# Optimization experiments

Hardware: AMD Instinct MI355X
Metric: run time of the kernel (lower is better)

The kernel has to match this reference:

```python
import jax, jax.numpy as jnp
import numpy as np

NUM_HEADS = 32
NEG_INF = -1e9


def setup_inputs() -> dict:
    key = jax.random.key(0)
    ks = jax.random.split(key, 7)
    B, S, H = 8, 4, 4096
    hd = H // NUM_HEADS
    position = 4096
    max_seq = position + S  # 4100
    sc = H ** -0.5  # keep projection outputs O(1)
    return {
        "hidden_states": jax.random.normal(ks[0], (B, S, H), jnp.float32),
        "Wq": jax.random.normal(ks[1], (H, H), jnp.float32) * sc,
        "Wk": jax.random.normal(ks[2], (H, H), jnp.float32) * sc,
        "Wv": jax.random.normal(ks[3], (H, H), jnp.float32) * sc,
        "Wo": jax.random.normal(ks[4], (H, H), jnp.float32) * sc,
        "key_cache": jax.random.normal(ks[5], (B, NUM_HEADS, max_seq, hd), jnp.float32),
        "value_cache": jax.random.normal(ks[6], (B, NUM_HEADS, max_seq, hd), jnp.float32),
        "position": position,
    }


def reference(hidden_states, Wq, Wk, Wv, Wo, key_cache, value_cache, position):
    B, S, H = hidden_states.shape
    nh = NUM_HEADS
    hd = H // nh
    scale = hd ** -0.5

    def proj(x, W):  # nn.Linear: x @ W.T -> [B, nh, S, hd]
        return (x @ W.T).reshape(B, S, nh, hd).transpose(0, 2, 1, 3)

    q = proj(hidden_states, Wq)
    k = proj(hidden_states, Wk)
    v = proj(hidden_states, Wv)

    # KV-cache slice update (position is a static Python int)
    key_cache = jax.lax.dynamic_update_slice(key_cache, k, (0, 0, position, 0))
    value_cache = jax.lax.dynamic_update_slice(value_cache, v, (0, 0, position, 0))

    kv_len = position + S
    k_all = key_cache[:, :, :kv_len, :]   # [B, nh, kv_len, hd]
    v_all = value_cache[:, :, :kv_len, :]

    scores = jnp.einsum('bhsd,bhtd->bhst', q, k_all) * scale  # [B, nh, S, kv_len]
    # triu(ones(S, kv_len), diagonal=position+1): mask col t when t > position + s
    mask = jnp.arange(kv_len)[None, :] > (position + jnp.arange(S))[:, None]
    scores = jnp.where(mask, NEG_INF, scores)
    attn = jax.nn.softmax(scores, axis=-1)

    out = jnp.einsum('bhst,bhtd->bhsd', attn, v_all)
    out = out.transpose(0, 2, 1, 3).reshape(B, S, H)
    return out @ Wo.T
```

## Files before the change

### kernel.cpp

```cpp
#include <hip/hip_runtime.h>
#include <cstdint>

#define HDIM   4096
#define NHEADS 32
#define HDH    128
#define BB     8
#define SQ     4
#define MAXSEQ 4100
#define QSCALE 0.08838834764831845f

#define PKCH  64
#define PLSTR 68
#define KSPL  512

__device__ __forceinline__ void dot4(float& a, const float4& p, const float4& q) {
    a = fmaf(p.x, q.x, fmaf(p.y, q.y, fmaf(p.z, q.z, fmaf(p.w, q.w, a))));
}

__global__ __launch_bounds__(256) void proj_split(
    const float* __restrict__ X,
    const float* __restrict__ W0, const float* __restrict__ W1, const float* __restrict__ W2,
    float* __restrict__ P)
{
    __shared__ float Wt[128][PLSTR];
    __shared__ float Xt[32][PLSTR];
    const float* __restrict__ W = (blockIdx.z == 0) ? W0 : ((blockIdx.z == 1) ? W1 : W2);
    const int tid = threadIdx.x;
    const int c0 = blockIdx.x * 128;
    const int kbase = blockIdx.y * KSPL;
    const int cg = tid & 31;
    const int rg = tid >> 5;

    float acc[4][4];
    #pragma unroll
    for (int r = 0; r < 4; ++r)
        #pragma unroll
        for (int j = 0; j < 4; ++j) acc[r][j] = 0.f;

    for (int ch = 0; ch < KSPL; ch += PKCH) {
        const int k0 = kbase + ch;
        #pragma unroll
        for (int i = 0; i < 8; ++i) {
            int fidx = (i << 8) + tid;
            int row = fidx >> 4;
            int kq = (fidx & 15) << 2;
            *(float4*)&Wt[row][kq] = *(const float4*)&W[(size_t)(c0 + row) * HDIM + k0 + kq];
        }
        #pragma unroll
        for (int i = 0; i < 2; ++i) {
            int fidx = (i << 8) + tid;
            int row = fidx >> 4;
            int kq = (fidx & 15) << 2;
            *(float4*)&Xt[row][kq] = *(const float4*)&X[(size_t)row * HDIM + k0 + kq];
        }
        __syncthreads();
        #pragma unroll 4
        for (int k = 0; k < PKCH; k += 4) {
            float4 w0 = *(const float4*)&Wt[cg][k];
            float4 w1 = *(const float4*)&Wt[cg + 32][k];
            float4 w2 = *(const float4*)&Wt[cg + 64][k];
            float4 w3 = *(const float4*)&Wt[cg + 96][k];
            float4 x0 = *(const float4*)&Xt[rg * 4 + 0][k];
            float4 x1 = *(const float4*)&Xt[rg * 4 + 1][k];
            float4 x2 = *(const float4*)&Xt[rg * 4 + 2][k];
            float4 x3 = *(const float4*)&Xt[rg * 4 + 3][k];
            dot4(acc[0][0], x0, w0); dot4(acc[0][1], x0, w1); dot4(acc[0][2], x0, w2); dot4(acc[0][3], x0, w3);
            dot4(acc[1][0], x1, w0); dot4(acc[1][1], x1, w1); dot4(acc[1][2], x1, w2); dot4(acc[1][3], x1, w3);
            dot4(acc[2][0], x2, w0); dot4(acc[2][1], x2, w1); dot4(acc[2][2], x2, w2); dot4(acc[2][3], x2, w3);
            dot4(acc[3][0], x3, w0); dot4(acc[3][1], x3, w1); dot4(acc[3][2], x3, w2); dot4(acc[3][3], x3, w3);
        }
        __syncthreads();
    }

    float* __restrict__ Pp = P + (size_t)(blockIdx.z * gridDim.y + blockIdx.y) * 32 * HDIM;
    #pragma unroll
    for (int r = 0; r < 4; ++r)
        #pragma unroll
        for (int j = 0; j < 4; ++j)
            Pp[(size_t)(rg * 4 + r) * HDIM + c0 + j * 32 + cg] = acc[r][j];
}

__global__ __launch_bounds__(256) void reduce_qkv(
    const float* __restrict__ P, float* __restrict__ qw,
    float* __restrict__ kw, float* __restrict__ vw)
{
    const int idx = blockIdx.x * 256 + threadIdx.x;
    const int mat = idx >> 17;
    const int rc = idx & 131071;
    const float* p = P + (size_t)mat * 1048576 + rc;
    float s = 0.f;
    #pragma unroll
    for (int i = 0; i < 8; ++i) s += p[(size_t)i * 131072];
    const int r = rc >> 12, c = rc & 4095;
    const int b = r >> 2, si = r & 3, h = c >> 7, d = c & 127;
    const size_t o = ((size_t)(b * NHEADS + h) * SQ + si) * HDH + d;
    if (mat == 0)      qw[o] = s * QSCALE;
    else if (mat == 1) kw[o] = s;
    else               vw[o] = s;
}

__global__ __launch_bounds__(256) void reduce_out(
    const float* __restrict__ P, float* __restrict__ out)
{
    const int idx = blockIdx.x * 256 + threadIdx.x;
    float s = 0.f;
    #pragma unroll
    for (int i = 0; i < 8; ++i) s += P[(size_t)i * 131072 + idx];
    out[idx] = s;
}

__device__ __forceinline__ float tree_reduce4(float p0, float p1, float p2, float p3, int li) {
    float a = (li & 16) ? p1 : p0;
    float b = (li & 16) ? p0 : p1;
    a += __shfl_xor(b, 16);
    float c = (li & 16) ? p3 : p2;
    float d = (li & 16) ? p2 : p3;
    c += __shfl_xor(d, 16);
    float e = (li & 8) ? c : a;
    float f = (li & 8) ? a : c;
    e += __shfl_xor(f, 8);
    e += __shfl_xor(e, 4);
    e += __shfl_xor(e, 2);
    e += __shfl_xor(e, 1);
    return e;
}

__global__ __launch_bounds__(1024) void attn_kernel(
    const float* __restrict__ kc, const float* __restrict__ vc,
    const float* __restrict__ qw, const float* __restrict__ kw,
    const float* __restrict__ vw, float* __restrict__ ow,
    const int* __restrict__ posp)
{
    __shared__ __align__(16) float sc[MAXSEQ * 4];
    __shared__ __align__(16) float o_part[16][SQ][HDH];
    __shared__ float wmax[16][4];
    __shared__ float l_part[16][4];
    __shared__ float m_fin[4], l_fin[4];

    const int bh = blockIdx.x;
    const int pos = *posp;
    const int kvlen = pos + SQ;
    const int pos_main = pos & ~31;
    const int tid = threadIdx.x;
    const int w = tid >> 6;
    const int lane = tid & 63;
    const int half = (lane >> 5) & 1;
    const int li = lane & 31;
    const int sg = ((li >> 3) & 1) * 2 + ((li >> 4) & 1);

    const float* __restrict__ qb = qw + (size_t)bh * 512 + li * 4;
    const float4 q0 = *(const float4*)(qb + 0);
    const float4 q1 = *(const float4*)(qb + 128);
    const float4 q2 = *(const float4*)(qb + 256);
    const float4 q3 = *(const float4*)(qb + 384);

    const float* __restrict__ kbase = kc + (size_t)bh * MAXSEQ * HDH + li * 4;
    const float* __restrict__ vbase = vc + (size_t)bh * MAXSEQ * HDH + li * 4;
    const float* __restrict__ knew = kw + (size_t)bh * 512 + li * 4;
    const float* __restrict__ vnew = vw + (size_t)bh * 512 + li * 4;

    float mloc = -1e30f;

    {
        int t = 2 * w + half;
        if (t < pos_main) {
            float4 kcur = *(const float4*)(kbase + (size_t)t * HDH);
            while (true) {
                const int tn = t + 32;
                const bool more = (tn < pos_main);
                float4 knx;
                if (more) knx = *(const float4*)(kbase + (size_t)tn * HDH);
                float p0 = fmaf(q0.x, kcur.x, fmaf(q0.y, kcur.y, fmaf(q0.z, kcur.z, q0.w * kcur.w)));
                float p1 = fmaf(q1.x, kcur.x, fmaf(q1.y, kcur.y, fmaf(q1.z, kcur.z, q1.w * kcur.w)));
                float p2 = fmaf(q2.x, kcur.x, fmaf(q2.y, kcur.y, fmaf(q2.z, kcur.z, q2.w * kcur.w)));
                float p3 = fmaf(q3.x, kcur.x, fmaf(q3.y, kcur.y, fmaf(q3.z, kcur.z, q3.w * kcur.w)));
                float e = tree_reduce4(p0, p1, p2, p3, li);
                mloc = fmaxf(mloc, e);
                if ((li & 7) == 0) sc[t * 4 + sg] = e;
                if (!more) break;
                kcur = knx; t = tn;
            }
        }
        for (int tt = pos_main + 2 * w + half; tt < kvlen; tt += 32) {
            const float* kr = (tt < pos) ? (kbase + (size_t)tt * HDH)
                                         : (knew + (size_t)(tt - pos) * HDH);
            float4 k4 = *(const float4*)kr;
            float p0 = fmaf(q0.x, k4.x, fmaf(q0.y, k4.y, fmaf(q0.z, k4.z, q0.w * k4.w)));
            float p1 = fmaf(q1.x, k4.x, fmaf(q1.y, k4.y, fmaf(q1.z, k4.z, q1.w * k4.w)));
            float p2 = fmaf(q2.x, k4.x, fmaf(q2.y, k4.y, fmaf(q2.z, k4.z, q2.w * k4.w)));
            float p3 = fmaf(q3.x, k4.x, fmaf(q3.y, k4.y, fmaf(q3.z, k4.z, q3.w * k4.w)));
            float e = tree_reduce4(p0, p1, p2, p3, li);
            if (tt > pos + sg) e = -1e9f;
            mloc = fmaxf(mloc, e);
            if ((li & 7) == 0) sc[tt * 4 + sg] = e;
        }
    }
    float mw = fmaxf(mloc, __shfl_xor(mloc, 32));
    if (lane < 32 && (li & 7) == 0) wmax[w][sg] = mw;
    __syncthreads();
    if (tid < 4) {
        float m = wmax[0][tid];
        #pragma unroll
        for (int i = 1; i < 16; ++i) m = fmaxf(m, wmax[i][tid]);
        m_fin[tid] = m;
    }
    __syncthreads();
    const float mf0 = m_fin[0], mf1 = m_fin[1], mf2 = m_fin[2], mf3 = m_fin[3];

    float lp0 = 0.f, lp1 = 0.f, lp2 = 0.f, lp3 = 0.f;
    for (int t = tid; t < kvlen; t += 1024) {
        float4 s4 = *(float4*)&sc[t * 4];
        s4.x = __expf(s4.x - mf0);
        s4.y = __expf(s4.y - mf1);
        s4.z = __expf(s4.z - mf2);
        s4.w = __expf(s4.w - mf3);
        *(float4*)&sc[t * 4] = s4;
        lp0 += s4.x; lp1 += s4.y; lp2 += s4.z; lp3 += s4.w;
    }
    #pragma unroll
    for (int off = 32; off; off >>= 1) {
        lp0 += __shfl_xor(lp0, off);
        lp1 += __shfl_xor(lp1, off);
        lp2 += __shfl_xor(lp2, off);
        lp3 += __shfl_xor(lp3, off);
    }
    if (lane == 0) { l_part[w][0] = lp0; l_part[w][1] = lp1; l_part[w][2] = lp2; l_part[w][3] = lp3; }
    __syncthreads();
    if (tid < 4) {
        float L = 0.f;
        #pragma unroll
        for (int i = 0; i < 16; ++i) L += l_part[i][tid];
        l_fin[tid] = L;
    }

    float4 o0 = {0,0,0,0}, o1 = {0,0,0,0}, o2 = {0,0,0,0}, o3 = {0,0,0,0};
    {
        int t = 2 * w + half;
        if (t < pos_main) {
            float4 vcur = *(const float4*)(vbase + (size_t)t * HDH);
            while (true) {
                const int tn = t + 32;
                const bool more = (tn < pos_main);
                float4 vnx;
                if (more) vnx = *(const float4*)(vbase + (size_t)tn * HDH);
                float4 e4 = *(float4*)&sc[t * 4];
                o0.x = fmaf(e4.x, vcur.x, o0.x); o0.y = fmaf(e4.x, vcur.y, o0.y);
                o0.z = fmaf(e4.x, vcur.z, o0.z); o0.w = fmaf(e4.x, vcur.w, o0.w);
                o1.x = fmaf(e4.y, vcur.x, o1.x); o1.y = fmaf(e4.y, vcur.y, o1.y);
                o1.z = fmaf(e4.y, vcur.z, o1.z); o1.w = fmaf(e4.y, vcur.w, o1.w);
                o2.x = fmaf(e4.z, vcur.x, o2.x); o2.y = fmaf(e4.z, vcur.y, o2.y);
                o2.z = fmaf(e4.z, vcur.z, o2.z); o2.w = fmaf(e4.z, vcur.w, o2.w);
                o3.x = fmaf(e4.w, vcur.x, o3.x); o3.y = fmaf(e4.w, vcur.y, o3.y);
                o3.z = fmaf(e4.w, vcur.z, o3.z); o3.w = fmaf(e4.w, vcur.w, o3.w);
                if (!more) break;
                vcur = vnx; t = tn;
            }
        }
        for (int tt = pos_main + 2 * w + half; tt < kvlen; tt += 32) {
            const float* vr = (tt < pos) ? (vbase + (size_t)tt * HDH)
                                         : (vnew + (size_t)(tt - pos) * HDH);
            float4 v4 = *(const float4*)vr;
            float4 e4 = *(float4*)&sc[tt * 4];
            o0.x = fmaf(e4.x, v4.x, o0.x); o0.y = fmaf(e4.x, v4.y, o0.y);
            o0.z = fmaf(e4.x, v4.z, o0.z); o0.w = fmaf(e4.x, v4.w, o0.w);
            o1.x = fmaf(e4.y, v4.x, o1.x); o1.y = fmaf(e4.y, v4.y, o1.y);
            o1.z = fmaf(e4.y, v4.z, o1.z); o1.w = fmaf(e4.y, v4.w, o1.w);
            o2.x = fmaf(e4.z, v4.x, o2.x); o2.y = fmaf(e4.z, v4.y, o2.y);
            o2.z = fmaf(e4.z, v4.z, o2.z); o2.w = fmaf(e4.z, v4.w, o2.w);
            o3.x = fmaf(e4.w, v4.x, o3.x); o3.y = fmaf(e4.w, v4.y, o3.y);
            o3.z = fmaf(e4.w, v4.z, o3.z); o3.w = fmaf(e4.w, v4.w, o3.w);
        }
    }
    o0.x += __shfl_xor(o0.x, 32); o0.y += __shfl_xor(o0.y, 32);
    o0.z += __shfl_xor(o0.z, 32); o0.w += __shfl_xor(o0.w, 32);
    o1.x += __shfl_xor(o1.x, 32); o1.y += __shfl_xor(o1.y, 32);
    o1.z += __shfl_xor(o1.z, 32); o1.w += __shfl_xor(o1.w, 32);
    o2.x += __shfl_xor(o2.x, 32); o2.y += __shfl_xor(o2.y, 32);
    o2.z += __shfl_xor(o2.z, 32); o2.w += __shfl_xor(o2.w, 32);
    o3.x += __shfl_xor(o3.x, 32); o3.y += __shfl_xor(o3.y, 32);
    o3.z += __shfl_xor(o3.z, 32); o3.w += __shfl_xor(o3.w, 32);
    if (half == 0) {
        *(float4*)&o_part[w][0][li * 4] = o0;
        *(float4*)&o_part[w][1][li * 4] = o1;
        *(float4*)&o_part[w][2][li * 4] = o2;
        *(float4*)&o_part[w][3][li * 4] = o3;
    }
    __syncthreads();
    if (tid < 512) {
        const int s = tid >> 7, d = tid & 127;
        float a = 0.f;
        #pragma unroll
        for (int i = 0; i < 16; ++i) a += o_part[i][s][d];
        const int b = bh >> 5, h = bh & 31;
        ow[((size_t)(b * SQ + s) << 12) + (h << 7) + d] = a / l_fin[s];
    }
}

extern "C" void kernel_launch(void* const* d_in, const int* in_sizes, int n_in,
                              void* d_out, int out_size, void* d_ws, size_t ws_size,
                              hipStream_t stream) {
    const float* hs = (const float*)d_in[0];
    const float* Wq = (const float*)d_in[1];
    const float* Wk = (const float*)d_in[2];
    const float* Wv = (const float*)d_in[3];
    const float* Wo = (const float*)d_in[4];
    const float* kc = (const float*)d_in[5];
    const float* vc = (const float*)d_in[6];
    const int*  pos = (const int*)d_in[7];
    float* out = (float*)d_out;

    float* ws = (float*)d_ws;
    float* qw = ws;
    float* kw = ws + 131072;
    float* vw = ws + 262144;
    float* ow = ws + 393216;
    float* Pq = ws + 524288;
    float* Po = ws + 3670016;

    proj_split<<<dim3(32, 8, 3), 256, 0, stream>>>(hs, Wq, Wk, Wv, Pq);
    reduce_qkv<<<1536, 256, 0, stream>>>(Pq, qw, kw, vw);
    attn_kernel<<<256, 1024, 0, stream>>>(kc, vc, qw, kw, vw, ow, pos);
    proj_split<<<dim3(32, 8, 1), 256, 0, stream>>>(ow, Wo, Wo, Wo, Po);
    reduce_out<<<512, 256, 0, stream>>>(Po, out);
}
```

Measured before the change: 339.6 us.

## Fuse QKV split-K reduction into attention kernel and deepen KV prefetch

Removes the separate reduce_qkv launch. Each attention block now sums the eight split-K partials for its own head's q, k and v directly from the projection workspace into shared memory, and the new k/v rows are read from LDS instead of global buffers. It also changes the K and V streaming loops from a one-ahead to a two-ahead register prefetch to hide more memory latency. This saves a launch and the round trip of writing and re-reading q/k/v. In exchange it adds extra LDS, register pressure and a serial reduction prologue at the start of every attention block.

```diff
diff --git a/kernel.cpp b/kernel.cpp
--- a/kernel.cpp
+++ b/kernel.cpp
@@ -80,25 +80,6 @@
             Pp[(size_t)(rg * 4 + r) * HDIM + c0 + j * 32 + cg] = acc[r][j];
 }
 
-__global__ __launch_bounds__(256) void reduce_qkv(
-    const float* __restrict__ P, float* __restrict__ qw,
-    float* __restrict__ kw, float* __restrict__ vw)
-{
-    const int idx = blockIdx.x * 256 + threadIdx.x;
-    const int mat = idx >> 17;
-    const int rc = idx & 131071;
-    const float* p = P + (size_t)mat * 1048576 + rc;
-    float s = 0.f;
-    #pragma unroll
-    for (int i = 0; i < 8; ++i) s += p[(size_t)i * 131072];
-    const int r = rc >> 12, c = rc & 4095;
-    const int b = r >> 2, si = r & 3, h = c >> 7, d = c & 127;
-    const size_t o = ((size_t)(b * NHEADS + h) * SQ + si) * HDH + d;
-    if (mat == 0)      qw[o] = s * QSCALE;
-    else if (mat == 1) kw[o] = s;
-    else               vw[o] = s;
-}
-
 __global__ __launch_bounds__(256) void reduce_out(
     const float* __restrict__ P, float* __restrict__ out)
 {
@@ -127,12 +108,14 @@
 
 __global__ __launch_bounds__(1024) void attn_kernel(
     const float* __restrict__ kc, const float* __restrict__ vc,
-    const float* __restrict__ qw, const float* __restrict__ kw,
-    const float* __restrict__ vw, float* __restrict__ ow,
+    const float* __restrict__ Pq, float* __restrict__ ow,
     const int* __restrict__ posp)
 {
     __shared__ __align__(16) float sc[MAXSEQ * 4];
     __shared__ __align__(16) float o_part[16][SQ][HDH];
+    __shared__ __align__(16) float qs_lds[SQ * HDH];
+    __shared__ __align__(16) float ks_lds[SQ * HDH];
+    __shared__ __align__(16) float vs_lds[SQ * HDH];
     __shared__ float wmax[16][4];
     __shared__ float l_part[16][4];
     __shared__ float m_fin[4], l_fin[4];
@@ -148,43 +131,64 @@
     const int li = lane & 31;
     const int sg = ((li >> 3) & 1) * 2 + ((li >> 4) & 1);
 
-    const float* __restrict__ qb = qw + (size_t)bh * 512 + li * 4;
-    const float4 q0 = *(const float4*)(qb + 0);
-    const float4 q1 = *(const float4*)(qb + 128);
-    const float4 q2 = *(const float4*)(qb + 256);
-    const float4 q3 = *(const float4*)(qb + 384);
+    {
+        const int b = bh >> 5, h = bh & 31;
+        if (tid < 512) {
+            const int s = tid >> 7, d = tid & 127;
+            const size_t base = (size_t)(b * SQ + s) * HDIM + h * HDH + d;
+            float a = 0.f;
+            #pragma unroll
+            for (int i = 0; i < 8; ++i) a += Pq[(size_t)i * 131072 + base];
+            qs_lds[tid] = a * QSCALE;
+        } else {
+            const int u = tid - 512;
+            const int s = u >> 7, d = u & 127;
+            const size_t base = (size_t)(b * SQ + s) * HDIM + h * HDH + d;
+            float ak = 0.f, av = 0.f;
+            #pragma unroll
+            for (int i = 0; i < 8; ++i) {
+                ak += Pq[(size_t)(8 + i) * 131072 + base];
+                av += Pq[(size_t)(16 + i) * 131072 + base];
+            }
+            ks_lds[u] = ak;
+            vs_lds[u] = av;
+        }
+    }
+    __syncthreads();
+
+    const float4 q0 = *(const float4*)&qs_lds[0 * HDH + li * 4];
+    const float4 q1 = *(const float4*)&qs_lds[1 * HDH + li * 4];
+    const float4 q2 = *(const float4*)&qs_lds[2 * HDH + li * 4];
+    const float4 q3 = *(const float4*)&qs_lds[3 * HDH + li * 4];
 
     const float* __restrict__ kbase = kc + (size_t)bh * MAXSEQ * HDH + li * 4;
     const float* __restrict__ vbase = vc + (size_t)bh * MAXSEQ * HDH + li * 4;
-    const float* __restrict__ knew = kw + (size_t)bh * 512 + li * 4;
-    const float* __restrict__ vnew = vw + (size_t)bh * 512 + li * 4;
 
     float mloc = -1e30f;
 
     {
-        int t = 2 * w + half;
-        if (t < pos_main) {
-            float4 kcur = *(const float4*)(kbase + (size_t)t * HDH);
-            while (true) {
-                const int tn = t + 32;
-                const bool more = (tn < pos_main);
-                float4 knx;
-                if (more) knx = *(const float4*)(kbase + (size_t)tn * HDH);
-                float p0 = fmaf(q0.x, kcur.x, fmaf(q0.y, kcur.y, fmaf(q0.z, kcur.z, q0.w * kcur.w)));
-                float p1 = fmaf(q1.x, kcur.x, fmaf(q1.y, kcur.y, fmaf(q1.z, kcur.z, q1.w * kcur.w)));
-                float p2 = fmaf(q2.x, kcur.x, fmaf(q2.y, kcur.y, fmaf(q2.z, kcur.z, q2.w * kcur.w)));
-                float p3 = fmaf(q3.x, kcur.x, fmaf(q3.y, kcur.y, fmaf(q3.z, kcur.z, q3.w * kcur.w)));
+        const int t0 = 2 * w + half;
+        if (t0 < pos_main) {
+            float4 ka = *(const float4*)(kbase + (size_t)t0 * HDH);
+            float4 kb;
+            if (t0 + 32 < pos_main) kb = *(const float4*)(kbase + (size_t)(t0 + 32) * HDH);
+            for (int t = t0; t < pos_main; t += 32) {
+                float4 kn;
+                if (t + 64 < pos_main) kn = *(const float4*)(kbase + (size_t)(t + 64) * HDH);
+                float p0 = fmaf(q0.x, ka.x, fmaf(q0.y, ka.y, fmaf(q0.z, ka.z, q0.w * ka.w)));
+                float p1 = fmaf(q1.x, ka.x, fmaf(q1.y, ka.y, fmaf(q1.z, ka.z, q1.w * ka.w)));
+                float p2 = fmaf(q2.x, ka.x, fmaf(q2.y, ka.y, fmaf(q2.z, ka.z, q2.w * ka.w)));
+                float p3 = fmaf(q3.x, ka.x, fmaf(q3.y, ka.y, fmaf(q3.z, ka.z, q3.w * ka.w)));
                 float e = tree_reduce4(p0, p1, p2, p3, li);
                 mloc = fmaxf(mloc, e);
                 if ((li & 7) == 0) sc[t * 4 + sg] = e;
-                if (!more) break;
-                kcur = knx; t = tn;
+                ka = kb; kb = kn;
             }
         }
         for (int tt = pos_main + 2 * w + half; tt < kvlen; tt += 32) {
-            const float* kr = (tt < pos) ? (kbase + (size_t)tt * HDH)
-                                         : (knew + (size_t)(tt - pos) * HDH);
-            float4 k4 = *(const float4*)kr;
+            float4 k4;
+            if (tt < pos) k4 = *(const float4*)(kbase + (size_t)tt * HDH);
+            else          k4 = *(const float4*)&ks_lds[(tt - pos) * HDH + li * 4];
             float p0 = fmaf(q0.x, k4.x, fmaf(q0.y, k4.y, fmaf(q0.z, k4.z, q0.w * k4.w)));
             float p1 = fmaf(q1.x, k4.x, fmaf(q1.y, k4.y, fmaf(q1.z, k4.z, q1.w * k4.w)));
             float p2 = fmaf(q2.x, k4.x, fmaf(q2.y, k4.y, fmaf(q2.z, k4.z, q2.w * k4.w)));
@@ -235,31 +239,30 @@
 
     float4 o0 = {0,0,0,0}, o1 = {0,0,0,0}, o2 = {0,0,0,0}, o3 = {0,0,0,0};
     {
-        int t = 2 * w + half;
-        if (t < pos_main) {
-            float4 vcur = *(const float4*)(vbase + (size_t)t * HDH);
-            while (true) {
-                const int tn = t + 32;
-                const bool more = (tn < pos_main);
-                float4 vnx;
-                if (more) vnx = *(const float4*)(vbase + (size_t)tn * HDH);
+        const int t0 = 2 * w + half;
+        if (t0 < pos_main) {
+            float4 va = *(const float4*)(vbase + (size_t)t0 * HDH);
+            float4 vb;
+            if (t0 + 32 < pos_main) vb = *(const float4*)(vbase + (size_t)(t0 + 32) * HDH);
+            for (int t = t0; t < pos_main; t += 32) {
+                float4 vn;
+                if (t + 64 < pos_main) vn = *(const float4*)(vbase + (size_t)(t + 64) * HDH);
                 float4 e4 = *(float4*)&sc[t * 4];
-                o0.x = fmaf(e4.x, vcur.x, o0.x); o0.y = fmaf(e4.x, vcur.y, o0.y);
-                o0.z = fmaf(e4.x, vcur.z, o0.z); o0.w = fmaf(e4.x, vcur.w, o0.w);
-                o1.x = fmaf(e4.y, vcur.x, o1.x); o1.y = fmaf(e4.y, vcur.y, o1.y);
-                o1.z = fmaf(e4.y, vcur.z, o1.z); o1.w = fmaf(e4.y, vcur.w, o1.w);
-                o2.x = fmaf(e4.z, vcur.x, o2.x); o2.y = fmaf(e4.z, vcur.y, o2.y);
-                o2.z = fmaf(e4.z, vcur.z, o2.z); o2.w = fmaf(e4.z, vcur.w, o2.w);
-                o3.x = fmaf(e4.w, vcur.x, o3.x); o3.y = fmaf(e4.w, vcur.y, o3.y);
-                o3.z = fmaf(e4.w, vcur.z, o3.z); o3.w = fmaf(e4.w, vcur.w, o3.w);
-                if (!more) break;
-                vcur = vnx; t = tn;
+                o0.x = fmaf(e4.x, va.x, o0.x); o0.y = fmaf(e4.x, va.y, o0.y);
+                o0.z = fmaf(e4.x, va.z, o0.z); o0.w = fmaf(e4.x, va.w, o0.w);
+                o1.x = fmaf(e4.y, va.x, o1.x); o1.y = fmaf(e4.y, va.y, o1.y);
+                o1.z = fmaf(e4.y, va.z, o1.z); o1.w = fmaf(e4.y, va.w, o1.w);
+                o2.x = fmaf(e4.z, va.x, o2.x); o2.y = fmaf(e4.z, va.y, o2.y);
+                o2.z = fmaf(e4.z, va.z, o2.z); o2.w = fmaf(e4.z, va.w, o2.w);
+                o3.x = fmaf(e4.w, va.x, o3.x); o3.y = fmaf(e4.w, va.y, o3.y);
+                o3.z = fmaf(e4.w, va.z, o3.z); o3.w = fmaf(e4.w, va.w, o3.w);
+                va = vb; vb = vn;
             }
         }
         for (int tt = pos_main + 2 * w + half; tt < kvlen; tt += 32) {
-            const float* vr = (tt < pos) ? (vbase + (size_t)tt * HDH)
-                                         : (vnew + (size_t)(tt - pos) * HDH);
-            float4 v4 = *(const float4*)vr;
+            float4 v4;
+            if (tt < pos) v4 = *(const float4*)(vbase + (size_t)tt * HDH);
+            else          v4 = *(const float4*)&vs_lds[(tt - pos) * HDH + li * 4];
             float4 e4 = *(float4*)&sc[tt * 4];
             o0.x = fmaf(e4.x, v4.x, o0.x); o0.y = fmaf(e4.x, v4.y, o0.y);
             o0.z = fmaf(e4.x, v4.z, o0.z); o0.w = fmaf(e4.x, v4.w, o0.w);
@@ -310,16 +313,12 @@
     float* out = (float*)d_out;
 
     float* ws = (float*)d_ws;
-    float* qw = ws;
-    float* kw = ws + 131072;
-    float* vw = ws + 262144;
-    float* ow = ws + 393216;
-    float* Pq = ws + 524288;
-    float* Po = ws + 3670016;
+    float* ow = ws;
+    float* Pq = ws + 131072;
+    float* Po = ws + 3276800;
 
     proj_split<<<dim3(32, 8, 3), 256, 0, stream>>>(hs, Wq, Wk, Wv, Pq);
-    reduce_qkv<<<1536, 256, 0, stream>>>(Pq, qw, kw, vw);
-    attn_kernel<<<256, 1024, 0, stream>>>(kc, vc, qw, kw, vw, ow, pos);
+    attn_kernel<<<256, 1024, 0, stream>>>(kc, vc, Pq, ow, pos);
     proj_split<<<dim3(32, 8, 1), 256, 0, stream>>>(ow, Wo, Wo, Wo, Po);
     reduce_out<<<512, 256, 0, stream>>>(Po, out);
 }
```

After: 330.0 us. 1.03x faster.
